# Optimization experiments

Measured on AMD Instinct MI355X. Metric: run time of the kernel, lower is better.

## Reference

```python
import jax, jax.numpy as jnp
import numpy as np

EMBED = 512
HEADS = 8
QKV = 64
HEAD_DIM = QKV // HEADS  # 8


def setup_inputs() -> dict:
    key = jax.random.key(0)
    ks = jax.random.split(key, 10)
    B, S = 8, 2048
    s = 1.0 / np.sqrt(EMBED)
    inp = {
        "x": jax.random.normal(ks[0], (B, S, EMBED), dtype=jnp.float32),
        "mask_matrix": jnp.zeros((S, S), dtype=jnp.float32),
        "Wq": jax.random.uniform(ks[1], (EMBED, QKV), jnp.float32, -s, s),
        "bq": jax.random.uniform(ks[2], (QKV,), jnp.float32, -s, s),
        "Wk": jax.random.uniform(ks[3], (EMBED, QKV), jnp.float32, -s, s),
        "bk": jax.random.uniform(ks[4], (QKV,), jnp.float32, -s, s),
        "Wv": jax.random.uniform(ks[5], (EMBED, QKV), jnp.float32, -s, s),
        "bv": jax.random.uniform(ks[6], (QKV,), jnp.float32, -s, s),
        "Wu": jax.random.uniform(ks[7], (QKV, EMBED), jnp.float32, -1.0 / 8.0, 1.0 / 8.0),
        "bu": jax.random.uniform(ks[8], (EMBED,), jnp.float32, -1.0 / 8.0, 1.0 / 8.0),
    }
    return inp


def reference(x, mask_matrix, Wq, bq, Wk, bk, Wv, bv, Wu, bu):
    B, S, _ = x.shape
    # projections to fixed 64-dim
    Q = x @ Wq + bq  # [B,S,64]
    K = x @ Wk + bk
    V = x @ Wv + bv
    # faithful reshape (NO head transpose, matching the original view chain)
    Q = Q.reshape(B * HEADS, S, HEAD_DIM)
    K = K.reshape(B * HEADS, S, HEAD_DIM)
    V = V.reshape(B * HEADS, S, HEAD_DIM)
    scores = jnp.einsum('gqd,gkd->gqk', Q, K)  # [B*H,S,S]
    scores = (scores + mask_matrix[None, :, :]) / np.sqrt(HEAD_DIM)
    probs = jax.nn.softmax(scores, axis=2)
    attn = jnp.einsum('gqk,gkd->gqd', probs, V)  # [B*H,S,hd]
    attn = attn.reshape(B, S, HEADS * HEAD_DIM)
    return attn @ Wu + bu
```

## Files before the change

kernel.cpp:

```cpp
#include <hip/hip_runtime.h>

typedef float f32x4 __attribute__((ext_vector_type(4)));
typedef float f32x16 __attribute__((ext_vector_type(16)));
typedef short s16x8 __attribute__((ext_vector_type(8)));
typedef unsigned int u32x2 __attribute__((ext_vector_type(2)));
typedef unsigned int u32x4 __attribute__((ext_vector_type(4)));

#define DEVFN static __device__ __forceinline__

constexpr int S_ = 2048;
constexpr int E_ = 512;
constexpr int D_ = 8;
constexpr int P_ = 64;
constexpr float C2 = 0.35355339059327373f * 1.4426950408889634f;


constexpr size_t FLAGA_OFF = 0;
constexpr size_t WT_OFF    = 1024;
constexpr size_t WUT_OFF   = WT_OFF + (size_t)192 * 512 * 2;
constexpr size_t QG_OFF    = WUT_OFF + (size_t)512 * 64 * 2;
constexpr size_t KG_OFF    = QG_OFF + (size_t)64 * 2048 * 8 * 2;
constexpr size_t VTG_OFF   = KG_OFF + (size_t)64 * 2048 * 8 * 2;

DEVFN short f2bf(float f) {
  unsigned u = __builtin_bit_cast(unsigned, f);
  return (short)((u + 0x7FFFu + ((u >> 16) & 1u)) >> 16);
}

DEVFN unsigned pkbf(float lo, float hi) {
  unsigned r;
  asm("v_cvt_pk_bf16_f32 %0, %1, %2" : "=v"(r) : "v"(lo), "v"(hi));
  return r;
}

DEVFN float fexp2(float x) {
#if __has_builtin(__builtin_amdgcn_exp2f)
  return __builtin_amdgcn_exp2f(x);
#else
  return exp2f(x);
#endif
}

DEVFN f32x16 mfma32(s16x8 a, s16x8 b, f32x16 c) {
  return __builtin_amdgcn_mfma_f32_32x32x16_bf16(a, b, c, 0, 0, 0);
}

DEVFN f32x16 zero16() {
  f32x16 z = {0,0,0,0,0,0,0,0,0,0,0,0,0,0,0,0};
  return z;
}

__global__ __launch_bounds__(256)
void prep_kernel(const float* __restrict__ Wq, const float* __restrict__ Wk,
                 const float* __restrict__ Wv, const float* __restrict__ Wu,
                 const float* __restrict__ maskm, short* __restrict__ WT,
                 short* __restrict__ WUT, int* __restrict__ flagA)
{
  int bid = blockIdx.x, tid = threadIdx.x;
  if (bid < 48) {
    int base = (bid * 256 + tid) * 8;
#pragma unroll
    for (int j = 0; j < 8; ++j) {
      int idx = base + j;
      int n = idx >> 9, k = idx & 511;
      const float* W = (n < 64) ? Wq : ((n < 128) ? Wk : Wv);
      WT[idx] = f2bf(W[k * 64 + (n & 63)]);
    }
  } else if (bid < 56) {
    int base = ((bid - 48) * 256 + tid) * 16;
#pragma unroll
    for (int j = 0; j < 16; ++j) {
      int idx = base + j;
      int n = idx >> 6, k = idx & 63;
      WUT[idx] = f2bf(Wu[k * 512 + n]);
    }
  } else {
    __shared__ int bf_;
    if (tid == 0) bf_ = 0;
    __syncthreads();
    const f32x4* m4 = (const f32x4*)maskm;
    int base = (bid - 56) * 4096;
    unsigned any = 0;
#pragma unroll
    for (int i = 0; i < 16; ++i) {
      f32x4 v = m4[base + i * 256 + tid];
      any |= __builtin_bit_cast(unsigned, v[0]) | __builtin_bit_cast(unsigned, v[1])
           | __builtin_bit_cast(unsigned, v[2]) | __builtin_bit_cast(unsigned, v[3]);
    }
    if (any != 0) atomicOr(&bf_, 1);
    __syncthreads();
    if (tid == 0) flagA[bid - 56] = bf_;
  }
}

__global__ __launch_bounds__(384)
void proj_kernel(const float* __restrict__ x, const short* __restrict__ WT,
                 const float* __restrict__ bq, const float* __restrict__ bk,
                 const float* __restrict__ bv, short* __restrict__ QG,
                 short* __restrict__ KG, short* __restrict__ VTG)
{
  __shared__ short xl[32 * 520];
  int tid = threadIdx.x;
  int mb = blockIdx.x * 32;
  for (int i = tid; i < 32 * 128; i += 384) {
    int row = i >> 7, c4 = i & 127;
    f32x4 v = *(const f32x4*)(x + (size_t)(mb + row) * E_ + c4 * 4);
    u32x2 w;
    w[0] = pkbf(v[0], v[1]);
    w[1] = pkbf(v[2], v[3]);
    *(u32x2*)(&xl[row * 520 + c4 * 4]) = w;
  }
  __syncthreads();
  int lane = tid & 63, wvi = tid >> 6;
  int l31 = lane & 31, h = lane >> 5;
  int nstrip = wvi * 32;
  f32x16 acc = zero16();
#pragma unroll 4
  for (int kk = 0; kk < E_; kk += 16) {
    s16x8 af = *(const s16x8*)(WT + (size_t)(nstrip + l31) * E_ + kk + 8 * h);
    s16x8 bf = *(const s16x8*)(&xl[l31 * 520 + kk + 8 * h]);
    acc = mfma32(af, bf, acc);
  }
  int token = mb + l31;
  int bidx = token >> 11, s = token & 2047;
  int gg = bidx * 8 + (s >> 8);
#pragma unroll
  for (int i = 0; i < 4; ++i) {
    int n0 = nstrip + 8 * i + 4 * h;
    int proj = n0 >> 6;
    int wi = n0 & 63;
    int head = wi >> 3, db = wi & 7;
    const float* bias = (proj == 0) ? bq : ((proj == 1) ? bk : bv);
    float sc = (proj == 0) ? C2 : 1.0f;
    float f0 = (acc[4*i+0] + bias[wi+0]) * sc;
    float f1 = (acc[4*i+1] + bias[wi+1]) * sc;
    float f2 = (acc[4*i+2] + bias[wi+2]) * sc;
    float f3 = (acc[4*i+3] + bias[wi+3]) * sc;
    int p = ((s & 255) << 3) + head;
    if (proj == 2) {
      int k16 = p & 15;
      int slot = (k16 & 3) + ((k16 >> 2) & 1) * 8 + (k16 >> 3) * 4;
      size_t vb = (size_t)gg * (S_ * D_) + (size_t)(p >> 4) * 128 + slot;
      VTG[vb + (db+0)*16] = f2bf(f0);
      VTG[vb + (db+1)*16] = f2bf(f1);
      VTG[vb + (db+2)*16] = f2bf(f2);
      VTG[vb + (db+3)*16] = f2bf(f3);
    } else {
      short* dst = (proj == 0) ? QG : KG;
      u32x2 o;
      o[0] = pkbf(f0, f1);
      o[1] = pkbf(f2, f3);
      *(u32x2*)(dst + ((size_t)gg * S_ + p) * D_ + db) = o;
    }
  }
}

#define PAIR_BODY(kb, PREFETCH, USEMASK)                                \
  {                                                                     \
    f32x16 st0 = mfma32(kf0, qf, zero16());                             \
    f32x16 st1 = mfma32(kf1, qf, zero16());                             \
    s16x8 va0a = *(const s16x8*)vptr;                                   \
    s16x8 va0b = *(const s16x8*)(vptr + 144);                           \
    s16x8 va1a = *(const s16x8*)(vptr + 288);                           \
    s16x8 va1b = *(const s16x8*)(vptr + 432);                           \
    vptr += 576;                                                        \
    if (PREFETCH) {                                                     \
      kf0 = *(const s16x8*)kptr;                                        \
      kf1 = *(const s16x8*)(kptr + kstride);                            \
      kptr += 2 * kstride;                                              \
    }                                                                   \
    float p0[16], p1[16];                                               \
    _Pragma("unroll")                                                   \
    for (int r = 0; r < 16; ++r) {                                      \
      float s0 = st0[r], s1 = st1[r];                                   \
      if (USEMASK) {                                                    \
        int key = (kb) + (r & 3) + 8 * (r >> 2) + 4 * h;                \
        s0 += maskm[(size_t)q * S_ + key] * C2;                         \
        s1 += maskm[(size_t)q * S_ + key + 32] * C2;                    \
      }                                                                 \
      p0[r] = fexp2(s0);                                                \
      p1[r] = fexp2(s1);                                                \
    }                                                                   \
    u32x4 b00, b01, b10, b11;                                           \
    b00[0] = pkbf(p0[0],  p0[1]);  b00[1] = pkbf(p0[2],  p0[3]);        \
    b00[2] = pkbf(p0[4],  p0[5]);  b00[3] = pkbf(p0[6],  p0[7]);        \
    b01[0] = pkbf(p0[8],  p0[9]);  b01[1] = pkbf(p0[10], p0[11]);       \
    b01[2] = pkbf(p0[12], p0[13]); b01[3] = pkbf(p0[14], p0[15]);       \
    b10[0] = pkbf(p1[0],  p1[1]);  b10[1] = pkbf(p1[2],  p1[3]);        \
    b10[2] = pkbf(p1[4],  p1[5]);  b10[3] = pkbf(p1[6],  p1[7]);        \
    b11[0] = pkbf(p1[8],  p1[9]);  b11[1] = pkbf(p1[10], p1[11]);       \
    b11[2] = pkbf(p1[12], p1[13]); b11[3] = pkbf(p1[14], p1[15]);       \
    __builtin_amdgcn_s_setprio(1);                                      \
    acc = mfma32(va0a, __builtin_bit_cast(s16x8, b00), acc);            \
    acc = mfma32(va0b, __builtin_bit_cast(s16x8, b01), acc);            \
    acc = mfma32(va1a, __builtin_bit_cast(s16x8, b10), acc);            \
    acc = mfma32(va1b, __builtin_bit_cast(s16x8, b11), acc);            \
    __builtin_amdgcn_s_setprio(0);                                      \
  }

__global__ __launch_bounds__(512, 4)
void attn_kernel(const short* __restrict__ QG, const short* __restrict__ KG,
                 const short* __restrict__ VTG, const float* __restrict__ maskm,
                 const int* __restrict__ flagA, const short* __restrict__ WUT,
                 const float* __restrict__ bu, float* __restrict__ out)
{
  __shared__ short K_lds[S_ * D_];
  __shared__ short V_lds[128 * 9 * 16];
  __shared__ short A_lds[32 * 68];
  __shared__ short Z_lds[8];
  __shared__ int   sm_flag;
  int bid = blockIdx.x;
  int swz = (bid & 7) * 64 + (bid >> 3);
  int g  = swz >> 3;
  int qb = (swz & 7) * 256;
  int tid = threadIdx.x;
  {
    const u32x4* ks = (const u32x4*)(KG  + (size_t)g * (S_ * D_));
    const u32x4* vs = (const u32x4*)(VTG + (size_t)g * (S_ * D_));
    u32x4* kd = (u32x4*)K_lds;
#pragma unroll
    for (int it = 0; it < 4; ++it) {
      int i = tid + it * 512;
      kd[i] = ks[i];
      u32x4 v = vs[i];
      int t = i >> 4, rem = i & 15;
      *(u32x4*)(&V_lds[t * 144 + rem * 8]) = v;
    }
    if (tid < 8) Z_lds[tid] = 0;
    unsigned one2 = 0x3F803F80u;
    u32x2 o2; o2[0] = one2; o2[1] = one2;
    int t = tid >> 2, qr = tid & 3;
    *(u32x2*)(&V_lds[t * 144 + 128 + qr * 4]) = o2;
    if (tid < 64) {
      const u32x4* fa4 = (const u32x4*)flagA;
      u32x4 f = fa4[tid];
      unsigned anyf = f[0] | f[1] | f[2] | f[3];
      unsigned long long bb = __ballot(anyf != 0);
      if (tid == 0) sm_flag = (bb != 0ull) ? 1 : 0;
    }
  }
  __syncthreads();

  int lane = tid & 63, wvi = tid >> 6;
  int l31 = lane & 31, h = lane >> 5;
  int q = qb + wvi * 32 + l31;
  bool hi = (h != 0);
  int dcl = (l31 < 8) ? l31 : 8;
  s16x8 zero8 = {0,0,0,0,0,0,0,0};

  s16x8 qf = hi ? zero8
                : *(const s16x8*)(QG + ((size_t)g * S_ + q) * D_);
  const short* kptr = hi ? Z_lds : &K_lds[l31 * 8];
  int kstride = hi ? 0 : 32 * 8;
  const short* vptr = &V_lds[dcl * 16 + 8 * h];
  f32x16 acc = zero16();
  bool usemask = (sm_flag != 0);

  s16x8 kf0 = *(const s16x8*)kptr;
  s16x8 kf1 = *(const s16x8*)(kptr + kstride);
  kptr += 2 * kstride;

  if (!usemask) {
    for (int kb = 0; kb < S_ - 64; kb += 64) PAIR_BODY(kb, true, false)
    PAIR_BODY(S_ - 64, false, false)
  } else {
    for (int kb = 0; kb < S_ - 64; kb += 64) PAIR_BODY(kb, true, true)
    PAIR_BODY(S_ - 64, false, true)
  }
  float d0 = acc[4];
  float dp = __shfl_xor(d0, 32, 64);
  float den = hi ? dp : d0;
  float inv = __builtin_amdgcn_rcpf(den);
  u32x2 o;
  o[0] = pkbf(acc[0] * inv, acc[1] * inv);
  o[1] = pkbf(acc[2] * inv, acc[3] * inv);
  int local = wvi * 4 + (l31 >> 3);
  int col = (l31 & 7) * 8 + 4 * h;
  *(u32x2*)(&A_lds[local * 68 + col]) = o;
  __syncthreads();
  int nb = wvi * 64;
  f32x16 accA = zero16(), accB = zero16();
#pragma unroll
  for (int kk = 0; kk < 64; kk += 16) {
    s16x8 af  = *(const s16x8*)(&A_lds[l31 * 68 + kk + 8 * h]);
    s16x8 bfA = *(const s16x8*)(WUT + (size_t)(nb + l31) * P_ + kk + 8 * h);
    s16x8 bfB = *(const s16x8*)(WUT + (size_t)(nb + 32 + l31) * P_ + kk + 8 * h);
    accA = mfma32(af, bfA, accA);
    accB = mfma32(af, bfB, accB);
  }
  size_t token_base = (size_t)(g >> 3) * S_ + (g & 7) * 256 + (qb >> 3);
  size_t obase = token_base * E_;
  int nA = nb + l31, nB = nb + 32 + l31;
  float biasA = bu[nA], biasB = bu[nB];
#pragma unroll
  for (int r = 0; r < 16; ++r) {
    int m = (r & 3) + 8 * (r >> 2) + 4 * h;
    out[obase + (size_t)m * E_ + nA] = accA[r] + biasA;
    out[obase + (size_t)m * E_ + nB] = accB[r] + biasB;
  }
}

extern "C" void kernel_launch(void* const* d_in, const int* in_sizes, int n_in,
                              void* d_out, int out_size, void* d_ws, size_t ws_size,
                              hipStream_t stream) {
  const float* x     = (const float*)d_in[0];
  const float* maskm = (const float*)d_in[1];
  const float* Wq    = (const float*)d_in[2];
  const float* bq    = (const float*)d_in[3];
  const float* Wk    = (const float*)d_in[4];
  const float* bk    = (const float*)d_in[5];
  const float* Wv    = (const float*)d_in[6];
  const float* bv    = (const float*)d_in[7];
  const float* Wu    = (const float*)d_in[8];
  const float* bu    = (const float*)d_in[9];
  float* out = (float*)d_out;
  char* ws = (char*)d_ws;
  int*   flagA = (int*)(ws + FLAGA_OFF);
  short* WT    = (short*)(ws + WT_OFF);
  short* WUT   = (short*)(ws + WUT_OFF);
  short* QG    = (short*)(ws + QG_OFF);
  short* KG    = (short*)(ws + KG_OFF);
  short* VTG   = (short*)(ws + VTG_OFF);

  prep_kernel<<<312, 256, 0, stream>>>(Wq, Wk, Wv, Wu, maskm, WT, WUT, flagA);
  proj_kernel<<<512, 384, 0, stream>>>(x, WT, bq, bk, bv, QG, KG, VTG);
  attn_kernel<<<512, 512, 0, stream>>>(QG, KG, VTG, maskm, flagA, WUT, bu, out);
}
```

Measured before the change: 65.91 us.

## Read K from global memory and shrink LDS footprint to raise attention occupancy

The attention kernel no longer stages K in shared memory. K fragments are loaded directly from global memory (L2-cached), and a zeroed global buffer stands in for the padded lanes. V is copied unpadded, and the all-ones row for the softmax denominator moves to a small separate LDS array addressed through per-lane pointers. The LDS cut lets launch bounds target 8 blocks per CU instead of 4. In exchange, every K fragment becomes a global load per iteration, adding latency and cache traffic, and the tighter register budget may cause spills.

```diff
diff --git a/kernel.cpp b/kernel.cpp
--- a/kernel.cpp
+++ b/kernel.cpp
@@ -16,7 +16,8 @@
 
 
 constexpr size_t FLAGA_OFF = 0;
-constexpr size_t WT_OFF    = 1024;
+constexpr size_t ZERO_OFF  = 1024;
+constexpr size_t WT_OFF    = 2048;
 constexpr size_t WUT_OFF   = WT_OFF + (size_t)192 * 512 * 2;
 constexpr size_t QG_OFF    = WUT_OFF + (size_t)512 * 64 * 2;
 constexpr size_t KG_OFF    = QG_OFF + (size_t)64 * 2048 * 8 * 2;
@@ -54,9 +55,11 @@
 void prep_kernel(const float* __restrict__ Wq, const float* __restrict__ Wk,
                  const float* __restrict__ Wv, const float* __restrict__ Wu,
                  const float* __restrict__ maskm, short* __restrict__ WT,
-                 short* __restrict__ WUT, int* __restrict__ flagA)
+                 short* __restrict__ WUT, int* __restrict__ flagA,
+                 int* __restrict__ zerog)
 {
   int bid = blockIdx.x, tid = threadIdx.x;
+  if (bid == 0 && tid < 8) zerog[tid] = 0;
   if (bid < 48) {
     int base = (bid * 256 + tid) * 8;
 #pragma unroll
@@ -159,11 +162,11 @@
   {                                                                     \
     f32x16 st0 = mfma32(kf0, qf, zero16());                             \
     f32x16 st1 = mfma32(kf1, qf, zero16());                             \
-    s16x8 va0a = *(const s16x8*)vptr;                                   \
-    s16x8 va0b = *(const s16x8*)(vptr + 144);                           \
-    s16x8 va1a = *(const s16x8*)(vptr + 288);                           \
-    s16x8 va1b = *(const s16x8*)(vptr + 432);                           \
-    vptr += 576;                                                        \
+    s16x8 va0a = *(const s16x8*)vp0;                                    \
+    s16x8 va0b = *(const s16x8*)vp1;                                    \
+    s16x8 va1a = *(const s16x8*)vp2;                                    \
+    s16x8 va1b = *(const s16x8*)vp3;                                    \
+    vp0 += vstep; vp1 += vstep; vp2 += vstep; vp3 += vstep;             \
     if (PREFETCH) {                                                     \
       kf0 = *(const s16x8*)kptr;                                        \
       kf1 = *(const s16x8*)(kptr + kstride);                            \
@@ -198,16 +201,16 @@
     __builtin_amdgcn_s_setprio(0);                                      \
   }
 
-__global__ __launch_bounds__(512, 4)
+__global__ __launch_bounds__(512, 8)
 void attn_kernel(const short* __restrict__ QG, const short* __restrict__ KG,
                  const short* __restrict__ VTG, const float* __restrict__ maskm,
                  const int* __restrict__ flagA, const short* __restrict__ WUT,
-                 const float* __restrict__ bu, float* __restrict__ out)
+                 const float* __restrict__ bu, float* __restrict__ out,
+                 const short* __restrict__ zerog)
 {
-  __shared__ short K_lds[S_ * D_];
-  __shared__ short V_lds[128 * 9 * 16];
+  __shared__ short V_lds[128 * 128];
+  __shared__ short ones16[16];
   __shared__ short A_lds[32 * 68];
-  __shared__ short Z_lds[8];
   __shared__ int   sm_flag;
   int bid = blockIdx.x;
   int swz = (bid & 7) * 64 + (bid >> 3);
@@ -215,22 +218,14 @@
   int qb = (swz & 7) * 256;
   int tid = threadIdx.x;
   {
-    const u32x4* ks = (const u32x4*)(KG  + (size_t)g * (S_ * D_));
     const u32x4* vs = (const u32x4*)(VTG + (size_t)g * (S_ * D_));
-    u32x4* kd = (u32x4*)K_lds;
+    u32x4* vd = (u32x4*)V_lds;
 #pragma unroll
     for (int it = 0; it < 4; ++it) {
       int i = tid + it * 512;
-      kd[i] = ks[i];
-      u32x4 v = vs[i];
-      int t = i >> 4, rem = i & 15;
-      *(u32x4*)(&V_lds[t * 144 + rem * 8]) = v;
-    }
-    if (tid < 8) Z_lds[tid] = 0;
-    unsigned one2 = 0x3F803F80u;
-    u32x2 o2; o2[0] = one2; o2[1] = one2;
-    int t = tid >> 2, qr = tid & 3;
-    *(u32x2*)(&V_lds[t * 144 + 128 + qr * 4]) = o2;
+      vd[i] = vs[i];
+    }
+    if (tid < 8) ((unsigned*)ones16)[tid] = 0x3F803F80u;
     if (tid < 64) {
       const u32x4* fa4 = (const u32x4*)flagA;
       u32x4 f = fa4[tid];
@@ -245,14 +240,20 @@
   int l31 = lane & 31, h = lane >> 5;
   int q = qb + wvi * 32 + l31;
   bool hi = (h != 0);
-  int dcl = (l31 < 8) ? l31 : 8;
   s16x8 zero8 = {0,0,0,0,0,0,0,0};
 
   s16x8 qf = hi ? zero8
                 : *(const s16x8*)(QG + ((size_t)g * S_ + q) * D_);
-  const short* kptr = hi ? Z_lds : &K_lds[l31 * 8];
+  const short* kptr = hi ? zerog : (KG + ((size_t)g * S_ + l31) * D_);
   int kstride = hi ? 0 : 32 * 8;
-  const short* vptr = &V_lds[dcl * 16 + 8 * h];
+  bool realv = (l31 < 8);
+  const short* vbase = realv ? &V_lds[l31 * 16 + 8 * h] : &ones16[8 * h];
+  int voff  = realv ? 128 : 0;
+  int vstep = 4 * voff;
+  const short* vp0 = vbase;
+  const short* vp1 = vbase + voff;
+  const short* vp2 = vbase + 2 * voff;
+  const short* vp3 = vbase + 3 * voff;
   f32x16 acc = zero16();
   bool usemask = (sm_flag != 0);
 
@@ -316,13 +317,15 @@
   float* out = (float*)d_out;
   char* ws = (char*)d_ws;
   int*   flagA = (int*)(ws + FLAGA_OFF);
+  int*   zerog = (int*)(ws + ZERO_OFF);
   short* WT    = (short*)(ws + WT_OFF);
   short* WUT   = (short*)(ws + WUT_OFF);
   short* QG    = (short*)(ws + QG_OFF);
   short* KG    = (short*)(ws + KG_OFF);
   short* VTG   = (short*)(ws + VTG_OFF);
 
-  prep_kernel<<<312, 256, 0, stream>>>(Wq, Wk, Wv, Wu, maskm, WT, WUT, flagA);
+  prep_kernel<<<312, 256, 0, stream>>>(Wq, Wk, Wv, Wu, maskm, WT, WUT, flagA, zerog);
   proj_kernel<<<512, 384, 0, stream>>>(x, WT, bq, bk, bv, QG, KG, VTG);
-  attn_kernel<<<512, 512, 0, stream>>>(QG, KG, VTG, maskm, flagA, WUT, bu, out);
-}
+  attn_kernel<<<512, 512, 0, stream>>>(QG, KG, VTG, maskm, flagA, WUT, bu, out,
+                                       (const short*)zerog);
+}
```

Result: slower. 143.5 us (+117.7%).
